# Kernel optimization log

Hardware: AMD Instinct MI355X
Metric: run time of the kernel (lower is better)

## Reference

```python
import jax, jax.numpy as jnp
import numpy as np

B, S, D, NH = 2, 1024, 512, 16  # batch, seq_len, d_model, num_heads (chunk size!)
C = D // NH  # number of chunks produced by torch split(num_heads, dim=-1)


def _split_heads(x):
    # torch: torch.stack(x.split(NH, dim=-1)) -> (C, B, S, NH), chunk i = cols [i*NH:(i+1)*NH]
    b, s, d = x.shape
    return jnp.moveaxis(x.reshape(b, s, C, NH), 2, 0)


def setup_inputs() -> dict:
    key = jax.random.key(0)
    ks = jax.random.split(key, 7)
    mk = lambda k, shp, scale=1.0: (jax.random.normal(k, shp, dtype=jnp.float32) * scale)
    return {
        "Q": mk(ks[0], (B, S, D)),
        "K": mk(ks[1], (B, S, D)),
        "V": mk(ks[2], (B, S, D)),
        "Wq": mk(ks[3], (D, D), D ** -0.5),
        "Wk": mk(ks[4], (D, D), D ** -0.5),
        "Wv": mk(ks[5], (D, D), D ** -0.5),
        "Wo": mk(ks[6], (D, D), D ** -0.5),
    }


def reference(Q, K, V, Wq, Wk, Wv, Wo):
    # bias-free linear projections (torch Linear: x @ W.T)
    q = Q @ Wq.T
    k = K @ Wk.T
    v = V @ Wv.T
    qh, kh, vh = _split_heads(q), _split_heads(k), _split_heads(v)  # (C, B, S, NH)
    # NOTE: scale is sqrt(Q.size(-1)) = sqrt(num_heads), faithful to source
    scale = jnp.sqrt(jnp.asarray(float(NH), dtype=qh.dtype))
    scores = jnp.einsum("cbmh,cbnh->cbmn", qh, kh) / scale  # (C, B, S, S)
    weights = jax.nn.softmax(scores, axis=-1)
    att = jnp.einsum("cbmn,cbnh->cbmh", weights, vh)  # (C, B, S, NH)
    # faithful to torch permute(0,2,1,3) then reshape(batch, -1, d_model)
    out = att.transpose(0, 2, 1, 3).reshape(B, -1, D)
    out = out @ Wo.T
    return (out, weights)
```

## Files before the change

### kernel.cpp

```cpp
#include <hip/hip_runtime.h>
#include <cstdint>
#include <cstddef>


typedef __attribute__((ext_vector_type(8)))  short    short8;
typedef __attribute__((ext_vector_type(4)))  float    f32x4;
typedef __attribute__((ext_vector_type(4)))  unsigned u32x4;

union FragU { u32x4 u; short8 s; };

__device__ __forceinline__ unsigned pk_bf16(float a, float b) {
    unsigned ua = __float_as_uint(a), ub = __float_as_uint(b);
    ua = (ua + 0x7fffu + ((ua >> 16) & 1u)) >> 16;
    ub = (ub + 0x7fffu + ((ub >> 16) & 1u)) >> 16;
    return ua | (ub << 16);
}
__device__ __forceinline__ unsigned short bf16_1(float a) {
    unsigned ua = __float_as_uint(a);
    return (unsigned short)((ua + 0x7fffu + ((ua >> 16) & 1u)) >> 16);
}

template <bool BF16OUT>
__device__ __forceinline__ void gemm_nt_mfma_body(const float* __restrict__ X,
                                                  const float* __restrict__ W,
                                                  void* __restrict__ Pout,
                                                  float wscale)
{
    __shared__ unsigned Xs[128 * 17 * 4];
    __shared__ unsigned Ws[64 * 17 * 4];
    const int t  = threadIdx.x;
    const int m0 = blockIdx.y << 7;
    const int n0 = blockIdx.x << 6;
    const int wave = t >> 6, lane = t & 63;
    const int ml = lane & 15;
    const int g  = lane >> 4;

    f32x4 acc[2][4] = {{{0,0,0,0},{0,0,0,0},{0,0,0,0},{0,0,0,0}},
                       {{0,0,0,0},{0,0,0,0},{0,0,0,0},{0,0,0,0}}};

#pragma unroll 1
    for (int st = 0; st < 4; ++st) {
        if (st) __syncthreads();
#pragma unroll
        for (int rep = 0; rep < 8; ++rep) {
            int f  = rep * 256 + t;
            int kf = f & 15, r = f >> 4;
            const float* xr = X + (size_t)(m0 + r) * 512 + st * 128 + kf * 8;
            float4 a = *(const float4*)xr;
            float4 b = *(const float4*)(xr + 4);
            unsigned* dx = &Xs[(r * 17 + kf) * 4];
            dx[0] = pk_bf16(a.x, a.y); dx[1] = pk_bf16(a.z, a.w);
            dx[2] = pk_bf16(b.x, b.y); dx[3] = pk_bf16(b.z, b.w);
        }
#pragma unroll
        for (int rep = 0; rep < 4; ++rep) {
            int f  = rep * 256 + t;
            int kf = f & 15, r = f >> 4;
            const float* wr = W + (size_t)(n0 + r) * 512 + st * 128 + kf * 8;
            float4 c = *(const float4*)wr;
            float4 d = *(const float4*)(wr + 4);
            unsigned* dw = &Ws[(r * 17 + kf) * 4];
            dw[0] = pk_bf16(c.x * wscale, c.y * wscale);
            dw[1] = pk_bf16(c.z * wscale, c.w * wscale);
            dw[2] = pk_bf16(d.x * wscale, d.y * wscale);
            dw[3] = pk_bf16(d.z * wscale, d.w * wscale);
        }
        __syncthreads();
#pragma unroll
        for (int ks = 0; ks < 4; ++ks) {
            const int kf = ks * 4 + g;
            FragU a0, a1;
            a0.u = *(const u32x4*)&Xs[((wave * 32 + ml) * 17 + kf) * 4];
            a1.u = *(const u32x4*)&Xs[((wave * 32 + 16 + ml) * 17 + kf) * 4];
#pragma unroll
            for (int nf = 0; nf < 4; ++nf) {
                FragU bw;
                bw.u = *(const u32x4*)&Ws[((nf * 16 + ml) * 17 + kf) * 4];
                acc[0][nf] = __builtin_amdgcn_mfma_f32_16x16x32_bf16(
                    a0.s, bw.s, acc[0][nf], 0, 0, 0);
                acc[1][nf] = __builtin_amdgcn_mfma_f32_16x16x32_bf16(
                    a1.s, bw.s, acc[1][nf], 0, 0, 0);
            }
        }
    }
#pragma unroll
    for (int af = 0; af < 2; ++af)
#pragma unroll
        for (int nf = 0; nf < 4; ++nf)
#pragma unroll
            for (int r = 0; r < 4; ++r) {
                const int m = m0 + wave * 32 + af * 16 + g * 4 + r;
                const size_t idx = (size_t)m * 512 + n0 + nf * 16 + ml;
                if (BF16OUT)
                    ((unsigned short*)Pout)[idx] = bf16_1(acc[af][nf][r]);
                else
                    ((float*)Pout)[idx] = acc[af][nf][r];
            }
}

__global__ __launch_bounds__(256, 2) void proj3_kernel(
    const float* __restrict__ Q, const float* __restrict__ K, const float* __restrict__ V,
    const float* __restrict__ Wq, const float* __restrict__ Wk, const float* __restrict__ Wv,
    unsigned short* __restrict__ q, unsigned short* __restrict__ k,
    unsigned short* __restrict__ v)
{
    const float* X; const float* W; unsigned short* P; float ws;
    if (blockIdx.z == 0)      { X = Q; W = Wq; P = q; ws = 0.25f; }
    else if (blockIdx.z == 1) { X = K; W = Wk; P = k; ws = 1.0f; }
    else                      { X = V; W = Wv; P = v; ws = 1.0f; }
    gemm_nt_mfma_body<true>(X, W, P, ws);
}

__global__ __launch_bounds__(256, 2) void outproj_kernel(
    const float* __restrict__ att, const float* __restrict__ Wo, float* __restrict__ out)
{
    gemm_nt_mfma_body<false>(att, Wo, out, 1.0f);
}

__global__ __launch_bounds__(512)
void attn_mfma_kernel(
    const unsigned short* __restrict__ q, const unsigned short* __restrict__ k,
    const unsigned short* __restrict__ v,
    float* __restrict__ wts, float* __restrict__ att)
{
    __shared__ unsigned ksF[64 * 128];
    __shared__ unsigned vsT[16][514];
    __shared__ unsigned pbuf[8][16][18];

    const int t     = threadIdx.x;
    const int bid   = blockIdx.x;
    const int strip = bid & 7;
    const int cb    = bid >> 3;
    const int b     = cb & 1;
    const int c     = cb >> 1;
    const int m0b   = strip << 7;

    const unsigned short* kb = k + (size_t)b * 524288 + c * 16;
    const unsigned short* vb = v + (size_t)b * 524288 + c * 16;

#pragma unroll
    for (int rep = 0; rep < 4; ++rep) {
        int f = rep * 512 + t;
        int n = f >> 1, gg = f & 1;
        u32x4 kv = *(const u32x4*)(kb + (size_t)n * 512 + gg * 8);
        *(u32x4*)&ksF[(n >> 4) * 128 + ((n & 15) + (gg << 4)) * 4] = kv;
    }
#pragma unroll
    for (int rep = 0; rep < 4; ++rep) {
        int f = rep * 512 + t;
        int p = f >> 2, hq = f & 3;
        uint2 a  = *(const uint2*)(vb + (size_t)(2 * p)     * 512 + hq * 4);
        uint2 bb = *(const uint2*)(vb + (size_t)(2 * p + 1) * 512 + hq * 4);
        vsT[hq * 4 + 0][p] = (a.x & 0xffffu) | (bb.x << 16);
        vsT[hq * 4 + 1][p] = (a.x >> 16) | (bb.x & 0xffff0000u);
        vsT[hq * 4 + 2][p] = (a.y & 0xffffu) | (bb.y << 16);
        vsT[hq * 4 + 3][p] = (a.y >> 16) | (bb.y & 0xffff0000u);
    }
    __syncthreads();

    const int wave = t >> 6, lane = t & 63;
    const int ml = lane & 15;
    const int g  = lane >> 4;
    const int m0w = m0b + wave * 16;

    FragU qf;
    if (g < 2) {
        qf.u = *(const u32x4*)(q + (size_t)b * 524288
                                 + (size_t)(m0w + ml) * 512 + c * 16 + g * 8);
    } else {
        qf.u = (u32x4){0, 0, 0, 0};
    }

    const f32x4 zero4 = {0.f, 0.f, 0.f, 0.f};

    float rs = 0.f;
#pragma unroll 1
    for (int nt = 0; nt < 64; ++nt) {
        FragU ka;
        if (lane < 32) ka.u = *(const u32x4*)&ksF[nt * 128 + lane * 4];
        else           ka.u = (u32x4){0, 0, 0, 0};
        f32x4 st = __builtin_amdgcn_mfma_f32_16x16x32_bf16(ka.s, qf.s, zero4, 0, 0, 0);
        rs += (__expf(st[0]) + __expf(st[1])) + (__expf(st[2]) + __expf(st[3]));
    }
    rs += __shfl_xor(rs, 16);
    rs += __shfl_xor(rs, 32);
    const float inv = 1.0f / rs;

    f32x4 acc = zero4;
    float* wrow = wts + (size_t)cb * 1048576 + (size_t)(m0w + ml) * 1024;
#pragma unroll 1
    for (int ntp = 0; ntp < 32; ++ntp) {
#pragma unroll
        for (int sub = 0; sub < 2; ++sub) {
            const int nt = ntp * 2 + sub;
            FragU ka;
            if (lane < 32) ka.u = *(const u32x4*)&ksF[nt * 128 + lane * 4];
            else           ka.u = (u32x4){0, 0, 0, 0};
            f32x4 st = __builtin_amdgcn_mfma_f32_16x16x32_bf16(ka.s, qf.s, zero4, 0, 0, 0);
            float w0 = __expf(st[0]) * inv;
            float w1 = __expf(st[1]) * inv;
            float w2 = __expf(st[2]) * inv;
            float w3 = __expf(st[3]) * inv;
            *(float4*)(wrow + nt * 16 + g * 4) = make_float4(w0, w1, w2, w3);
            unsigned* pb = &pbuf[wave][ml][sub * 8 + g * 2];
            pb[0] = pk_bf16(w0, w1);
            pb[1] = pk_bf16(w2, w3);
        }
        FragU pa, vf;
        pa.u = *(const u32x4*)&pbuf[wave][ml][g * 4];
        vf.u = *(const u32x4*)&vsT[ml][ntp * 16 + g * 4];
        acc = __builtin_amdgcn_mfma_f32_16x16x32_bf16(pa.s, vf.s, acc, 0, 0, 0);
    }

    const int b2 = c >> 4;
#pragma unroll
    for (int r = 0; r < 4; ++r) {
        const int m  = m0w + g * 4 + r;
        const int m2 = (c & 15) * 64 + (m >> 4);
        const int d2 = (m & 15) * 32 + b * 16 + ml;
        att[((size_t)b2 * 1024 + m2) * 512 + d2] = acc[r];
    }
}

extern "C" void kernel_launch(void* const* d_in, const int* in_sizes, int n_in,
                              void* d_out, int out_size, void* d_ws, size_t ws_size,
                              hipStream_t stream)
{
    (void)in_sizes; (void)n_in; (void)out_size; (void)ws_size;
    const float* Q  = (const float*)d_in[0];
    const float* K  = (const float*)d_in[1];
    const float* V  = (const float*)d_in[2];
    const float* Wq = (const float*)d_in[3];
    const float* Wk = (const float*)d_in[4];
    const float* Wv = (const float*)d_in[5];
    const float* Wo = (const float*)d_in[6];

    float* out = (float*)d_out;
    float* wts = out + 1048576;

    float* ws  = (float*)d_ws;
    unsigned short* q16 = (unsigned short*)ws;
    unsigned short* k16 = (unsigned short*)(ws + (1u << 19));
    unsigned short* v16 = (unsigned short*)(ws + (1u << 20));
    float* att = ws + 2 * (1u << 20);

    proj3_kernel<<<dim3(8, 16, 3), 256, 0, stream>>>(Q, K, V, Wq, Wk, Wv,
                                                     q16, k16, v16);
    attn_mfma_kernel<<<512, 512, 0, stream>>>(q16, k16, v16, wts, att);
    outproj_kernel<<<dim3(8, 16, 1), 256, 0, stream>>>(att, Wo, out);
}
```

Measured before the change: 97.56 us.

## Single-pass softmax with split-N waves and deferred normalization in attention

Removes the separate row-sum pass: each wave computes exp scores once, keeps them packed as bf16 in registers, accumulates unnormalized P·V, and normalizes at the end. Pairs of waves split the key dimension in half and exchange partial sums and accumulators through shared memory, and the grid doubles to 1024 blocks of 64-row strips. This halves score MFMA/exp work but stores weights rounded from bf16-packed exps, which loses output precision, and it adds register pressure from the 64-entry array.

```diff
diff --git a/kernel.cpp b/kernel.cpp
--- a/kernel.cpp
+++ b/kernel.cpp
@@ -126,14 +126,16 @@
     __shared__ unsigned ksF[64 * 128];
     __shared__ unsigned vsT[16][514];
     __shared__ unsigned pbuf[8][16][18];
+    __shared__ float    sumx[4][2][16];
+    __shared__ float    accx[4][16][16];
 
     const int t     = threadIdx.x;
     const int bid   = blockIdx.x;
-    const int strip = bid & 7;
-    const int cb    = bid >> 3;
+    const int strip = bid & 15;
+    const int cb    = bid >> 4;
     const int b     = cb & 1;
     const int c     = cb >> 1;
-    const int m0b   = strip << 7;
+    const int m0b   = strip << 6;
 
     const unsigned short* kb = k + (size_t)b * 524288 + c * 16;
     const unsigned short* vb = v + (size_t)b * 524288 + c * 16;
@@ -158,10 +160,12 @@
     }
     __syncthreads();
 
-    const int wave = t >> 6, lane = t & 63;
-    const int ml = lane & 15;
-    const int g  = lane >> 4;
-    const int m0w = m0b + wave * 16;
+    const int wave  = t >> 6, lane = t & 63;
+    const int ml    = lane & 15;
+    const int g     = lane >> 4;
+    const int pair  = wave >> 1;
+    const int nhalf = wave & 1;
+    const int m0w   = m0b + pair * 16;
 
     FragU qf;
     if (g < 2) {
@@ -174,51 +178,70 @@
     const f32x4 zero4 = {0.f, 0.f, 0.f, 0.f};
 
     float rs = 0.f;
-#pragma unroll 1
-    for (int nt = 0; nt < 64; ++nt) {
-        FragU ka;
-        if (lane < 32) ka.u = *(const u32x4*)&ksF[nt * 128 + lane * 4];
-        else           ka.u = (u32x4){0, 0, 0, 0};
-        f32x4 st = __builtin_amdgcn_mfma_f32_16x16x32_bf16(ka.s, qf.s, zero4, 0, 0, 0);
-        rs += (__expf(st[0]) + __expf(st[1])) + (__expf(st[2]) + __expf(st[3]));
-    }
-    rs += __shfl_xor(rs, 16);
-    rs += __shfl_xor(rs, 32);
-    const float inv = 1.0f / rs;
-
+    unsigned ep[64];
     f32x4 acc = zero4;
-    float* wrow = wts + (size_t)cb * 1048576 + (size_t)(m0w + ml) * 1024;
-#pragma unroll 1
-    for (int ntp = 0; ntp < 32; ++ntp) {
+#pragma unroll
+    for (int ip = 0; ip < 16; ++ip) {
 #pragma unroll
         for (int sub = 0; sub < 2; ++sub) {
-            const int nt = ntp * 2 + sub;
+            const int i  = ip * 2 + sub;
+            const int nt = nhalf * 32 + i;
             FragU ka;
             if (lane < 32) ka.u = *(const u32x4*)&ksF[nt * 128 + lane * 4];
             else           ka.u = (u32x4){0, 0, 0, 0};
             f32x4 st = __builtin_amdgcn_mfma_f32_16x16x32_bf16(ka.s, qf.s, zero4, 0, 0, 0);
-            float w0 = __expf(st[0]) * inv;
-            float w1 = __expf(st[1]) * inv;
-            float w2 = __expf(st[2]) * inv;
-            float w3 = __expf(st[3]) * inv;
-            *(float4*)(wrow + nt * 16 + g * 4) = make_float4(w0, w1, w2, w3);
+            float e0 = __expf(st[0]);
+            float e1 = __expf(st[1]);
+            float e2 = __expf(st[2]);
+            float e3 = __expf(st[3]);
+            rs += (e0 + e1) + (e2 + e3);
+            ep[i * 2]     = pk_bf16(e0, e1);
+            ep[i * 2 + 1] = pk_bf16(e2, e3);
             unsigned* pb = &pbuf[wave][ml][sub * 8 + g * 2];
-            pb[0] = pk_bf16(w0, w1);
-            pb[1] = pk_bf16(w2, w3);
-        }
+            pb[0] = ep[i * 2];
+            pb[1] = ep[i * 2 + 1];
+        }
+        const int ntg = nhalf * 16 + ip;
         FragU pa, vf;
         pa.u = *(const u32x4*)&pbuf[wave][ml][g * 4];
-        vf.u = *(const u32x4*)&vsT[ml][ntp * 16 + g * 4];
+        vf.u = *(const u32x4*)&vsT[ml][ntg * 16 + g * 4];
         acc = __builtin_amdgcn_mfma_f32_16x16x32_bf16(pa.s, vf.s, acc, 0, 0, 0);
     }
 
-    const int b2 = c >> 4;
-#pragma unroll
-    for (int r = 0; r < 4; ++r) {
-        const int m  = m0w + g * 4 + r;
-        const int m2 = (c & 15) * 64 + (m >> 4);
-        const int d2 = (m & 15) * 32 + b * 16 + ml;
-        att[((size_t)b2 * 1024 + m2) * 512 + d2] = acc[r];
+    rs += __shfl_xor(rs, 16);
+    rs += __shfl_xor(rs, 32);
+    if (lane < 16) sumx[pair][nhalf][lane] = rs;
+    __syncthreads();
+    const float inv = 1.0f / (rs + sumx[pair][nhalf ^ 1][ml]);
+
+    if (nhalf) {
+#pragma unroll
+        for (int r = 0; r < 4; ++r) accx[pair][g * 4 + r][ml] = acc[r];
+    }
+    __syncthreads();
+
+    float* wrow = wts + (size_t)cb * 1048576 + (size_t)(m0w + ml) * 1024
+                      + nhalf * 512;
+#pragma unroll
+    for (int i = 0; i < 32; ++i) {
+        float a0 = __uint_as_float(ep[i * 2] << 16) * inv;
+        float a1 = __uint_as_float(ep[i * 2] & 0xffff0000u) * inv;
+        float a2 = __uint_as_float(ep[i * 2 + 1] << 16) * inv;
+        float a3 = __uint_as_float(ep[i * 2 + 1] & 0xffff0000u) * inv;
+        *(float4*)(wrow + i * 16 + g * 4) = make_float4(a0, a1, a2, a3);
+    }
+
+    if (!nhalf) {
+        const int b2 = c >> 4;
+#pragma unroll
+        for (int r = 0; r < 4; ++r) {
+            const float tot  = acc[r] + accx[pair][g * 4 + r][ml];
+            const float invr = __shfl(inv, g * 4 + r);
+            const int m  = m0w + g * 4 + r;
+            const int m2 = (c & 15) * 64 + (m >> 4);
+            const int d2 = (m & 15) * 32 + b * 16 + ml;
+            att[((size_t)b2 * 1024 + m2) * 512 + d2] = tot * invr;
+        }
     }
 }
 
@@ -246,6 +269,6 @@
 
     proj3_kernel<<<dim3(8, 16, 3), 256, 0, stream>>>(Q, K, V, Wq, Wk, Wv,
                                                      q16, k16, v16);
-    attn_mfma_kernel<<<512, 512, 0, stream>>>(q16, k16, v16, wts, att);
+    attn_mfma_kernel<<<1024, 512, 0, stream>>>(q16, k16, v16, wts, att);
     outproj_kernel<<<dim3(8, 16, 1), 256, 0, stream>>>(att, Wo, out);
 }
```

Result: slower. 128.0 us (+31.2%).
